# Optimization experiments

Hardware: AMD Instinct MI355X
Metric: run time of the kernel (lower is better)

## Reference

```python
import jax, jax.numpy as jnp
import numpy as np

DT = 0.01          # discretization timestep (init kwarg dt)
DAMP_MIN = 5e-4    # minimum damping (init kwarg damp_min)
BATCH, SEQ, D_IN, N_STATE = 16, 2048, 1024, 128


def setup_inputs() -> dict:
    key = jax.random.key(0)
    k1, k2, k3, k4, k5 = jax.random.split(key, 5)
    u = jax.random.normal(k1, (BATCH, SEQ, D_IN), jnp.float32)
    # A_real init: randn*0.1 - damp_min, then clamped to <= -damp_min (stability)
    A_real = jnp.minimum(jax.random.normal(k2, (N_STATE,), jnp.float32) * 0.1 - DAMP_MIN, -DAMP_MIN)
    A_imag = jax.random.normal(k3, (N_STATE,), jnp.float32)
    B = jax.random.normal(k4, (N_STATE, D_IN), jnp.float32) * 0.02
    C = jax.random.normal(k5, (D_IN, N_STATE), jnp.float32) * 0.02
    return {"u": u, "A_real": A_real, "A_imag": A_imag, "B": B, "C": C}


def reference(u, A_real, A_imag, B, C):
    """Real-input path of StableResonantSSM.

    Bilinear discretization of diagonal complex A:
      a_disc = (1 + dt/2 * a) / (1 - dt/2 * a)          (elementwise, A diagonal)
      B_disc = sqrt(dt) * B / (1 - dt/2 * a)            (row-wise scaling)
    Recurrence: h_t = a_disc * h_{t-1} + B_disc @ u_t;  y_t = Re(C @ h_t).
    """
    dt = jnp.float32(DT)
    a = (A_real + 1j * A_imag).astype(jnp.complex64)          # (N,)
    denom = 1.0 - (dt / 2) * a                                 # (N,) complex
    a_disc = (1.0 + (dt / 2) * a) / denom                      # (N,)
    B_disc = (jnp.sqrt(dt) * B.astype(jnp.complex64)) / denom[:, None]  # (N, D)

    # Precompute all input injections as one GEMM: (T, B, N) complex
    Bu = jnp.einsum('btd,nd->tbn', u, B_disc)

    def step(h, bu_t):
        h = a_disc * h + bu_t
        return h, h

    h0 = jnp.zeros((u.shape[0], a.shape[0]), jnp.complex64)
    _, hs = jax.lax.scan(step, h0, Bu)                         # hs: (T, B, N)

    # C is real, so Re(C @ h) == C @ Re(h)
    y = jnp.einsum('tbn,dn->btd', hs.real, C)                  # (B, T, D)
    return y
```

## Files before the change

kernel.cpp:

```cpp
#include <hip/hip_runtime.h>
#include <hip/hip_bf16.h>
#include <cstdint>

#define DT_F    0.01f
#define NB      16
#define T_SEQ   2048
#define DD      1024
#define NS      128
#define CHUNK   64
#define NCH     32

using f32x4  = __attribute__((ext_vector_type(4))) float;
using bf16x8 = __attribute__((ext_vector_type(8))) short;
using fl4    = __attribute__((ext_vector_type(4))) float;

#define AS1(p) ((const __attribute__((address_space(1))) void*)(p))
#define AS3(p) ((__attribute__((address_space(3))) void*)(p))

__device__ __forceinline__ unsigned short f2bf(float f) {
  union { float f; unsigned u; } v; v.f = f;
  unsigned r = v.u + 0x7fffu + ((v.u >> 16) & 1u);
  return (unsigned short)(r >> 16);
}
__device__ __forceinline__ float bf2f(unsigned short s) {
  union { unsigned u; float f; } v; v.u = ((unsigned)s) << 16;
  return v.f;
}
__device__ __forceinline__ unsigned short f2bf_hw(float f) {
  __hip_bfloat16 h = __float2bfloat16(f);
  return __builtin_bit_cast(unsigned short, h);
}

__device__ __forceinline__ void adisc_full(float Arn, float Ain,
                                           float& ar, float& ai,
                                           float& cr, float& ci) {
  const float dr = 1.f - 0.5f * DT_F * Arn;
  const float di = -0.5f * DT_F * Ain;
  const float inv = 1.f / (dr * dr + di * di);
  const float nr = 1.f + 0.5f * DT_F * Arn;
  const float nim = 0.5f * DT_F * Ain;
  ar = (nr * dr + nim * di) * inv;
  ai = (nim * dr - nr * di) * inv;
  const float s = sqrtf(DT_F);
  cr = s * dr * inv;
  ci = -s * di * inv;
}
__device__ __forceinline__ void adisc(float Arn, float Ain, float& ar, float& ai) {
  float cr, ci; adisc_full(Arn, Ain, ar, ai, cr, ci);
}

__global__ void prep_all(const float* __restrict__ B, const float* __restrict__ C,
                         unsigned short* __restrict__ Bb, unsigned short* __restrict__ Cb) {
  const int blk = blockIdx.x;
  const int tid = threadIdx.x;
  if (blk < 512) {
    const int i = blk * 256 + tid;
    Cb[i] = f2bf(C[i]);
  } else {
    const int i = (blk - 512) * 256 + tid;
    Bb[i] = f2bf(B[i]);
  }
}

__global__ __launch_bounds__(256, 2) void gemm1s(const float* __restrict__ U,
                                                 const float* __restrict__ Ar,
                                                 const float* __restrict__ Ai,
                                                 const unsigned short* __restrict__ Bb,
                                                 unsigned short* __restrict__ Hs,
                                                 float* __restrict__ F) {
  __shared__ __align__(16) char smem[24576];
  unsigned short* As = (unsigned short*)smem;
  unsigned short* Bs = (unsigned short*)(smem + 8192);
  char*           Bt = smem;

  const int tid  = threadIdx.x;
  const int lane = tid & 63;
  const int wave = tid >> 6;
  const int blk  = blockIdx.x;
  const size_t m0 = (size_t)blk * CHUNK;

  f32x4 acc[4][2];
  const f32x4 zero = {0.f, 0.f, 0.f, 0.f};
#pragma unroll
  for (int i = 0; i < 4; ++i)
#pragma unroll
    for (int j = 0; j < 2; ++j) acc[i][j] = zero;

  const int srow  = tid >> 2;
  const int scol  = (tid & 3) * 16;
  const int growl = lane >> 3;
  const int gcol  = (lane & 7) * 8;

  for (int k0 = 0; k0 < DD; k0 += 64) {
    __syncthreads();
#pragma unroll
    for (int g = 0; g < 4; ++g) {
      const int row = wave * 32 + g * 8;
      const unsigned short* gb = Bb + (size_t)(row + growl) * DD + k0 + gcol;
      __builtin_amdgcn_global_load_lds(AS1(gb), AS3(&Bs[row * 64]), 16, 0, 0);
    }
    {
      const float* ga = U + (m0 + srow) * DD + k0 + scol;
      fl4 v0 = *(const fl4*)ga;
      fl4 v1 = *(const fl4*)(ga + 4);
      fl4 v2 = *(const fl4*)(ga + 8);
      fl4 v3 = *(const fl4*)(ga + 12);
      bf16x8 p0, p1;
#pragma unroll
      for (int e = 0; e < 4; ++e) {
        p0[e] = (short)f2bf_hw(v0[e]); p0[4 + e] = (short)f2bf_hw(v1[e]);
        p1[e] = (short)f2bf_hw(v2[e]); p1[4 + e] = (short)f2bf_hw(v3[e]);
      }
      *(bf16x8*)&As[srow * 64 + scol]     = p0;
      *(bf16x8*)&As[srow * 64 + scol + 8] = p1;
    }
    __syncthreads();
#pragma unroll
    for (int ks = 0; ks < 2; ++ks) {
      bf16x8 af[4], bfr[2];
#pragma unroll
      for (int i = 0; i < 4; ++i)
        af[i] = *(const bf16x8*)&As[(i * 16 + (lane & 15)) * 64 + ks * 32 + (lane >> 4) * 8];
#pragma unroll
      for (int j = 0; j < 2; ++j)
        bfr[j] = *(const bf16x8*)&Bs[(wave * 32 + j * 16 + (lane & 15)) * 64 + ks * 32 + (lane >> 4) * 8];
#pragma unroll
      for (int i = 0; i < 4; ++i)
#pragma unroll
        for (int j = 0; j < 2; ++j)
          acc[i][j] = __builtin_amdgcn_mfma_f32_16x16x32_bf16(af[i], bfr[j], acc[i][j], 0, 0, 0);
    }
  }
  __syncthreads();

#pragma unroll
  for (int i = 0; i < 4; ++i) {
#pragma unroll
    for (int j = 0; j < 2; ++j) {
      const int n = wave * 32 + j * 16 + (lane & 15);
#pragma unroll
      for (int q = 0; q < 4; ++q) {
        const int t = i * 16 + (lane >> 4) * 4 + q;
        *(unsigned short*)(Bt + t * 256 + ((n * 2) ^ ((t & 7) << 4))) = f2bf_hw(acc[i][j][q]);
      }
    }
  }
  __syncthreads();

  if (tid < 128) {
    const int n = tid;
    float ar, ai, cr, ci; adisc_full(Ar[n], Ai[n], ar, ai, cr, ci);
    float hr = 0.f, hi = 0.f;
    unsigned short* o = Hs + (size_t)blk * (CHUNK * NS) + n;
#pragma unroll 8
    for (int t = 0; t < CHUNK; ++t) {
      const float s = bf2f(*(const unsigned short*)(Bt + t * 256 + ((n * 2) ^ ((t & 7) << 4))));
      const float br = cr * s;
      const float bi = ci * s;
      const float xr = fmaf(ar, hr, fmaf(-ai, hi, br));
      const float xi = fmaf(ar, hi, fmaf(ai, hr, bi));
      hr = xr; hi = xi;
      o[t * NS] = f2bf(hr);
    }
    F[(size_t)blk * 256 + n]       = hr;
    F[(size_t)blk * 256 + 128 + n] = hi;
  }
}

__global__ void carry_scan(const float* __restrict__ F,
                           const float* __restrict__ Ar, const float* __restrict__ Ai,
                           float* __restrict__ G) {
  const int b = blockIdx.x;
  const int n = threadIdx.x;
  float ar, ai; adisc(Ar[n], Ai[n], ar, ai);
  float alr = ar, ali = ai;
#pragma unroll
  for (int s = 0; s < 6; ++s) {
    const float tr = alr * alr - ali * ali;
    const float ti = 2.f * alr * ali;
    alr = tr; ali = ti;
  }
  float cr = 0.f, ci = 0.f;
  for (int c = 0; c < NCH; ++c) {
    const size_t idx = ((size_t)b * NCH + c) * 256 + n;
    G[idx]       = ar * cr - ai * ci;
    G[idx + 128] = ar * ci + ai * cr;
    const float fr = F[idx];
    const float fi = F[idx + 128];
    const float xr = fmaf(alr, cr, fmaf(-ali, ci, fr));
    const float xi = fmaf(alr, ci, fmaf(ali, cr, fi));
    cr = xr; ci = xi;
  }
}

__global__ __launch_bounds__(256, 2) void gemm2s(const unsigned short* __restrict__ Hs,
                                                 const float* __restrict__ G,
                                                 const float* __restrict__ Ar,
                                                 const float* __restrict__ Ai,
                                                 const unsigned short* __restrict__ Cb,
                                                 float* __restrict__ y) {
  __shared__ __align__(16) char Hl[64 * 256];
  const int tid  = threadIdx.x;
  const int lane = tid & 63;
  const int wave = tid >> 6;
  const int blk  = blockIdx.x;
  const int c    = blk & 31;
  const size_t m0 = (size_t)blk * CHUNK;

  const char* tile = (const char*)Hs + (size_t)blk * (CHUNK * NS * 2);
#pragma unroll
  for (int g = 0; g < 4; ++g) {
    const int r0 = wave * 16 + g * 4;
    const int r  = r0 + (lane >> 4);
    const int srcOff = r * 256 + ((((lane & 15)) * 16) ^ ((r & 7) << 4));
    __builtin_amdgcn_global_load_lds(AS1(tile + srcOff), AS3(Hl + r0 * 256), 16, 0, 0);
  }
  __syncthreads();

  if (c != 0 && tid < 128) {
    const int n = tid;
    float ar, ai; adisc(Ar[n], Ai[n], ar, ai);
    float gr = G[(size_t)blk * 256 + n];
    float gi = G[(size_t)blk * 256 + 128 + n];
#pragma unroll 8
    for (int t = 0; t < CHUNK; ++t) {
      unsigned short* pp = (unsigned short*)(Hl + t * 256 + ((n * 2) ^ ((t & 7) << 4)));
      *pp = f2bf(bf2f(*pp) + gr);
      const float xr = ar * gr - ai * gi;
      const float xi = ar * gi + ai * gr;
      gr = xr; gi = xi;
    }
  }
  __syncthreads();

  const f32x4 zero = {0.f, 0.f, 0.f, 0.f};
#pragma unroll
  for (int cg = 0; cg < 4; ++cg) {
    const int d0 = wave * 256 + cg * 64;
    f32x4 oacc[4][4];
#pragma unroll
    for (int i = 0; i < 4; ++i)
#pragma unroll
      for (int j = 0; j < 4; ++j) oacc[i][j] = zero;

#pragma unroll
    for (int ks = 0; ks < 4; ++ks) {
      bf16x8 af[4], bfr[4];
#pragma unroll
      for (int i = 0; i < 4; ++i) {
        const int r = i * 16 + (lane & 15);
        af[i] = *(const bf16x8*)(Hl + r * 256 + ((ks * 64 + (lane >> 4) * 16) ^ ((r & 7) << 4)));
      }
#pragma unroll
      for (int j = 0; j < 4; ++j)
        bfr[j] = *(const bf16x8*)(Cb + (size_t)(d0 + j * 16 + (lane & 15)) * NS + ks * 32 + (lane >> 4) * 8);
#pragma unroll
      for (int i = 0; i < 4; ++i)
#pragma unroll
        for (int j = 0; j < 4; ++j)
          oacc[i][j] = __builtin_amdgcn_mfma_f32_16x16x32_bf16(af[i], bfr[j], oacc[i][j], 0, 0, 0);
    }
#pragma unroll
    for (int i = 0; i < 4; ++i) {
      const size_t r0 = m0 + i * 16 + (lane >> 4) * 4;
#pragma unroll
      for (int j = 0; j < 4; ++j) {
        const int d = d0 + j * 16 + (lane & 15);
#pragma unroll
        for (int q = 0; q < 4; ++q)
          y[(r0 + q) * DD + d] = oacc[i][j][q];
      }
    }
  }
}

extern "C" void kernel_launch(void* const* d_in, const int* in_sizes, int n_in,
                              void* d_out, int out_size, void* d_ws, size_t ws_size,
                              hipStream_t stream) {
  const float* u  = (const float*)d_in[0];
  const float* Ar = (const float*)d_in[1];
  const float* Ai = (const float*)d_in[2];
  const float* B  = (const float*)d_in[3];
  const float* C  = (const float*)d_in[4];
  float* y = (float*)d_out;
  char* ws = (char*)d_ws;

  unsigned short* Bb = (unsigned short*)(ws);
  unsigned short* Cb = (unsigned short*)(ws + (256 << 10));
  float*          F  = (float*)(ws + (512 << 10));
  float*          G  = (float*)(ws + (1024 << 10));
  unsigned short* Hs = (unsigned short*)(ws + (1536 << 10));

  prep_all<<<dim3(1024), dim3(256), 0, stream>>>(B, C, Bb, Cb);
  gemm1s<<<dim3(NB * NCH), dim3(256), 0, stream>>>(u, Ar, Ai, Bb, Hs, F);
  carry_scan<<<dim3(NB), dim3(128), 0, stream>>>(F, Ar, Ai, G);
  gemm2s<<<dim3(NB * NCH), dim3(256), 0, stream>>>(Hs, G, Ar, Ai, Cb, y);
}
```

Measured before the change: 75.82 us.

## Swizzle GEMM1 LDS tiles and prefetch chunk finals into LDS in carry scan

The first GEMM now stores its A and B tiles in LDS with an XOR swizzle on 16-byte column groups, and the global_load_lds source addresses are permuted to match. This is meant to remove bank conflicts on the 128-byte-stride fragment reads feeding the MFMAs. Separately, the carry scan bulk-loads each batch's chunk-final states into shared memory with 256 threads using float4 loads, so the serial 32-step loop no longer waits on dependent global loads. The cost is extra index arithmetic and 32 KB of shared memory per carry block.

```diff
diff --git a/kernel.cpp b/kernel.cpp
--- a/kernel.cpp
+++ b/kernel.cpp
@@ -69,9 +69,9 @@
                                                  unsigned short* __restrict__ Hs,
                                                  float* __restrict__ F) {
   __shared__ __align__(16) char smem[24576];
-  unsigned short* As = (unsigned short*)smem;
-  unsigned short* Bs = (unsigned short*)(smem + 8192);
-  char*           Bt = smem;
+  char* As = smem;
+  char* Bs = smem + 8192;
+  char* Bt = smem;
 
   const int tid  = threadIdx.x;
   const int lane = tid & 63;
@@ -86,18 +86,20 @@
 #pragma unroll
     for (int j = 0; j < 2; ++j) acc[i][j] = zero;
 
-  const int srow  = tid >> 2;
-  const int scol  = (tid & 3) * 16;
+  const int srow = tid >> 2;
+  const int scol = (tid & 3) * 16;
+  const int sb0 = srow * 128 + (((tid & 3) * 32) ^ ((srow & 7) << 4));
+  const int sb1 = srow * 128 + ((((tid & 3) * 32) + 16) ^ ((srow & 7) << 4));
   const int growl = lane >> 3;
-  const int gcol  = (lane & 7) * 8;
+  const int gcolsw = 8 * ((lane & 7) ^ (lane >> 3));
 
   for (int k0 = 0; k0 < DD; k0 += 64) {
     __syncthreads();
 #pragma unroll
     for (int g = 0; g < 4; ++g) {
       const int row = wave * 32 + g * 8;
-      const unsigned short* gb = Bb + (size_t)(row + growl) * DD + k0 + gcol;
-      __builtin_amdgcn_global_load_lds(AS1(gb), AS3(&Bs[row * 64]), 16, 0, 0);
+      const unsigned short* gb = Bb + (size_t)(row + growl) * DD + k0 + gcolsw;
+      __builtin_amdgcn_global_load_lds(AS1(gb), AS3(Bs + row * 128), 16, 0, 0);
     }
     {
       const float* ga = U + (m0 + srow) * DD + k0 + scol;
@@ -111,19 +113,24 @@
         p0[e] = (short)f2bf_hw(v0[e]); p0[4 + e] = (short)f2bf_hw(v1[e]);
         p1[e] = (short)f2bf_hw(v2[e]); p1[4 + e] = (short)f2bf_hw(v3[e]);
       }
-      *(bf16x8*)&As[srow * 64 + scol]     = p0;
-      *(bf16x8*)&As[srow * 64 + scol + 8] = p1;
+      *(bf16x8*)(As + sb0) = p0;
+      *(bf16x8*)(As + sb1) = p1;
     }
     __syncthreads();
 #pragma unroll
     for (int ks = 0; ks < 2; ++ks) {
+      const int colb = ks * 64 + (lane >> 4) * 16;
       bf16x8 af[4], bfr[2];
 #pragma unroll
-      for (int i = 0; i < 4; ++i)
-        af[i] = *(const bf16x8*)&As[(i * 16 + (lane & 15)) * 64 + ks * 32 + (lane >> 4) * 8];
-#pragma unroll
-      for (int j = 0; j < 2; ++j)
-        bfr[j] = *(const bf16x8*)&Bs[(wave * 32 + j * 16 + (lane & 15)) * 64 + ks * 32 + (lane >> 4) * 8];
+      for (int i = 0; i < 4; ++i) {
+        const int r = i * 16 + (lane & 15);
+        af[i] = *(const bf16x8*)(As + r * 128 + (colb ^ ((r & 7) << 4)));
+      }
+#pragma unroll
+      for (int j = 0; j < 2; ++j) {
+        const int r = wave * 32 + j * 16 + (lane & 15);
+        bfr[j] = *(const bf16x8*)(Bs + r * 128 + (colb ^ ((r & 7) << 4)));
+      }
 #pragma unroll
       for (int i = 0; i < 4; ++i)
 #pragma unroll
@@ -170,26 +177,36 @@
 __global__ void carry_scan(const float* __restrict__ F,
                            const float* __restrict__ Ar, const float* __restrict__ Ai,
                            float* __restrict__ G) {
+  __shared__ float Fl[NCH * 256];
   const int b = blockIdx.x;
-  const int n = threadIdx.x;
-  float ar, ai; adisc(Ar[n], Ai[n], ar, ai);
-  float alr = ar, ali = ai;
-#pragma unroll
-  for (int s = 0; s < 6; ++s) {
-    const float tr = alr * alr - ali * ali;
-    const float ti = 2.f * alr * ali;
-    alr = tr; ali = ti;
-  }
-  float cr = 0.f, ci = 0.f;
-  for (int c = 0; c < NCH; ++c) {
-    const size_t idx = ((size_t)b * NCH + c) * 256 + n;
-    G[idx]       = ar * cr - ai * ci;
-    G[idx + 128] = ar * ci + ai * cr;
-    const float fr = F[idx];
-    const float fi = F[idx + 128];
-    const float xr = fmaf(alr, cr, fmaf(-ali, ci, fr));
-    const float xi = fmaf(alr, ci, fmaf(ali, cr, fi));
-    cr = xr; ci = xi;
+  const int tid = threadIdx.x;
+  const float4* src = (const float4*)(F + (size_t)b * NCH * 256);
+  float4* dst = (float4*)Fl;
+#pragma unroll
+  for (int i = 0; i < NCH * 64 / 256; ++i)
+    dst[tid + i * 256] = src[tid + i * 256];
+  __syncthreads();
+  if (tid < 128) {
+    const int n = tid;
+    float ar, ai; adisc(Ar[n], Ai[n], ar, ai);
+    float alr = ar, ali = ai;
+#pragma unroll
+    for (int s = 0; s < 6; ++s) {
+      const float tr = alr * alr - ali * ali;
+      const float ti = 2.f * alr * ali;
+      alr = tr; ali = ti;
+    }
+    float cr = 0.f, ci = 0.f;
+    for (int c = 0; c < NCH; ++c) {
+      const size_t idx = ((size_t)b * NCH + c) * 256 + n;
+      G[idx]       = ar * cr - ai * ci;
+      G[idx + 128] = ar * ci + ai * cr;
+      const float fr = Fl[c * 256 + n];
+      const float fi = Fl[c * 256 + 128 + n];
+      const float xr = fmaf(alr, cr, fmaf(-ali, ci, fr));
+      const float xi = fmaf(alr, ci, fmaf(ali, cr, fi));
+      cr = xr; ci = xi;
+    }
   }
 }
 
@@ -293,6 +310,6 @@
 
   prep_all<<<dim3(1024), dim3(256), 0, stream>>>(B, C, Bb, Cb);
   gemm1s<<<dim3(NB * NCH), dim3(256), 0, stream>>>(u, Ar, Ai, Bb, Hs, F);
-  carry_scan<<<dim3(NB), dim3(128), 0, stream>>>(F, Ar, Ai, G);
+  carry_scan<<<dim3(NB), dim3(256), 0, stream>>>(F, Ar, Ai, G);
   gemm2s<<<dim3(NB * NCH), dim3(256), 0, stream>>>(Hs, G, Ar, Ai, Cb, y);
 }
```

Result: faster. 73.78 us (-2.7%).
